# Optimization experiments

Hardware: AMD Instinct MI355X
Metric: run time of the kernel (lower is better)

The kernel has to match this reference:

```python
import jax, jax.numpy as jnp
import numpy as np

B, S, E, H = 4, 2048, 1024, 16
D = E // H
SCALE = np.sqrt(D).astype(np.float32)


def setup_inputs() -> dict:
    key = jax.random.key(0)
    ks = jax.random.split(key, 9)
    s = 1.0 / np.sqrt(E)
    return {
        "x": jax.random.normal(ks[0], (B, S, E), dtype=jnp.float32),
        "Wq": jax.random.uniform(ks[1], (E, E), jnp.float32, -s, s),
        "bq": jax.random.uniform(ks[2], (E,), jnp.float32, -s, s),
        "Wk": jax.random.uniform(ks[3], (E, E), jnp.float32, -s, s),
        "bk": jax.random.uniform(ks[4], (E,), jnp.float32, -s, s),
        "Wv": jax.random.uniform(ks[5], (E, E), jnp.float32, -s, s),
        "bv": jax.random.uniform(ks[6], (E,), jnp.float32, -s, s),
        "Wo": jax.random.uniform(ks[7], (E, E), jnp.float32, -s, s),
        "bo": jax.random.uniform(ks[8], (E,), jnp.float32, -s, s),
    }


def reference(x, Wq, bq, Wk, bk, Wv, bv, Wo, bo):
    # Linear projections (torch Linear: y = x @ W.T + b)
    q = x @ Wq.T + bq  # [B,S,E]
    k = x @ Wk.T + bk
    v = x @ Wv.T + bv
    # split heads -> [B,H,S,D]
    q = q.reshape(B, S, H, D).transpose(0, 2, 1, 3)
    k = k.reshape(B, S, H, D).transpose(0, 2, 1, 3)
    v = v.reshape(B, S, H, D).transpose(0, 2, 1, 3)
    scores = jnp.einsum("bhqd,bhkd->bhqk", q, k) / SCALE  # [B,H,S,S]
    attn = jax.nn.softmax(scores, axis=-1)  # dropout is identity at inference
    out = jnp.einsum("bhqk,bhkd->bhqd", attn, v)  # [B,H,S,D]
    out = out.transpose(0, 2, 1, 3).reshape(B, S, E)
    return out @ Wo.T + bo
```

## Files before the change

kernel.cpp:

```cpp
#include <hip/hip_runtime.h>
#include <math.h>

#define Bb 4
#define Ss 2048
#define Ee 1024
#define Hh 16
#define Dd 64

static constexpr int Mtot = Bb * Ss;
static constexpr size_t NK = (size_t)Ee * Ee;

typedef __bf16 bf16x8 __attribute__((ext_vector_type(8)));
typedef float  f32x16 __attribute__((ext_vector_type(16)));
typedef unsigned int uint32x2 __attribute__((ext_vector_type(2)));

extern "C" __device__ float __ocml_native_exp2_f32(float);

__device__ __forceinline__ unsigned short rne1(float x) {
  unsigned u = __float_as_uint(x);
  return (unsigned short)((u + 0x7FFFu + ((u >> 16) & 1u)) >> 16);
}
__device__ __forceinline__ short4 rne4(const float4 v) {
  short4 r;
  r.x = (short)rne1(v.x); r.y = (short)rne1(v.y);
  r.z = (short)rne1(v.z); r.w = (short)rne1(v.w);
  return r;
}

__global__ __launch_bounds__(256) void prep(const float* __restrict__ x,
                                            const float* __restrict__ wq,
                                            const float* __restrict__ wk,
                                            const float* __restrict__ wv,
                                            const float* __restrict__ wo,
                                            unsigned short* __restrict__ xb,
                                            unsigned short* __restrict__ wqkv,
                                            unsigned short* __restrict__ wob) {
  const int X4 = (int)((size_t)Mtot * Ee / 4);
  const int W4 = (int)(NK / 4);
  const int i = blockIdx.x * 256 + threadIdx.x;
  const float* src;
  unsigned short* dst;
  int off;
  if (i < X4) {
    src = x; dst = xb; off = i;
  } else {
    const int j = i - X4;
    const int seg = j >> 18;
    off = j & (W4 - 1);
    if (seg == 0)      { src = wq; dst = wqkv; }
    else if (seg == 1) { src = wk; dst = wqkv + NK; }
    else if (seg == 2) { src = wv; dst = wqkv + 2 * NK; }
    else               { src = wo; dst = wob; }
  }
  float4 v = ((const float4*)src)[off];
  ((short4*)dst)[off] = rne4(v);
}

__device__ __forceinline__ void gemm_core(const unsigned short* __restrict__ A,
                                          const unsigned short* __restrict__ W,
                                          unsigned short* sm, int bm, int bn,
                                          int tid, f32x16 acc[2][2]) {
  unsigned short* sA = sm;
  unsigned short* sW = sm + 9216;
  const int r  = tid >> 1;
  const int ch = (tid & 1) << 5;
  const int lane = tid & 63, w = tid >> 6;
  const int wm = (w & 1) << 6, wn = (w >> 1) << 6;
  const int m32 = lane & 31, g = lane >> 5;

  const unsigned short* A0 = A + (size_t)(bm + r) * Ee + ch;
  const unsigned short* W0 = W + (size_t)(bn + r) * Ee + ch;
  const int so = r * 72 + ch;

  for (int k0 = 0; k0 < Ee; k0 += 64) {
    uint4 a0 = *(const uint4*)(A0 + k0);
    uint4 a1 = *(const uint4*)(A0 + k0 + 8);
    uint4 a2 = *(const uint4*)(A0 + k0 + 16);
    uint4 a3 = *(const uint4*)(A0 + k0 + 24);
    uint4 w0 = *(const uint4*)(W0 + k0);
    uint4 w1 = *(const uint4*)(W0 + k0 + 8);
    uint4 w2 = *(const uint4*)(W0 + k0 + 16);
    uint4 w3 = *(const uint4*)(W0 + k0 + 24);
    __syncthreads();
    *(uint4*)(sA + so)      = a0; *(uint4*)(sA + so + 8)  = a1;
    *(uint4*)(sA + so + 16) = a2; *(uint4*)(sA + so + 24) = a3;
    *(uint4*)(sW + so)      = w0; *(uint4*)(sW + so + 8)  = w1;
    *(uint4*)(sW + so + 16) = w2; *(uint4*)(sW + so + 24) = w3;
    __syncthreads();
#pragma unroll
    for (int kk = 0; kk < 64; kk += 16) {
      const int kc = kk + (g << 3);
      bf16x8 af[2], wf[2];
#pragma unroll
      for (int s = 0; s < 2; ++s) {
        af[s] = *(const bf16x8*)(sA + (wm + (s << 5) + m32) * 72 + kc);
        wf[s] = *(const bf16x8*)(sW + (wn + (s << 5) + m32) * 72 + kc);
      }
#pragma unroll
      for (int si = 0; si < 2; ++si)
#pragma unroll
        for (int sj = 0; sj < 2; ++sj)
          acc[si][sj] = __builtin_amdgcn_mfma_f32_32x32x16_bf16(af[si], wf[sj], acc[si][sj], 0, 0, 0);
    }
  }
}


__global__ __launch_bounds__(256) void gemm_qkv(const unsigned short* __restrict__ xb,
                                                const unsigned short* __restrict__ wqkv,
                                                const float* __restrict__ bq,
                                                const float* __restrict__ bk,
                                                const float* __restrict__ bv,
                                                unsigned short* __restrict__ Qb,
                                                unsigned short* __restrict__ Kb,
                                                unsigned short* __restrict__ Vt) {
  __shared__ unsigned short sm[18432];
  f32x16 acc[2][2] = {};
  const int tid = threadIdx.x;
  const int bnIdx = blockIdx.x;
  const int bm = blockIdx.y << 7, bn = bnIdx << 7;
  gemm_core(xb, wqkv, sm, bm, bn, tid, acc);

  const int lane = tid & 63, w = tid >> 6;
  const int wm = (w & 1) << 6, wn = (w >> 1) << 6;
  const int m32 = lane & 31, g = lane >> 5;
  const int proj = bnIdx >> 3;
  const int cb   = (bnIdx & 7) << 7;
  const float* bp = proj == 0 ? bq : (proj == 1 ? bk : bv);
  const float SC = 0.18033688011112042f;

  if (proj == 2) {
    const int bmS = bm & (Ss - 1);
    const int b = bm >> 11;
#pragma unroll
    for (int si = 0; si < 2; ++si)
#pragma unroll
      for (int sj = 0; sj < 2; ++sj) {
        const int col = cb + wn + (sj << 5) + m32;
        const int hh = col >> 6, dd = col & 63;
        const float bvv = bp[col];
        unsigned short* vrow = Vt + ((size_t)((b * Hh + hh) * Dd + dd)) * Ss;
#pragma unroll
        for (int rq = 0; rq < 4; ++rq) {
          const int s0 = bmS + wm + (si << 5) + (g << 2) + (rq << 3);
          float4 v;
          v.x = acc[si][sj][rq * 4 + 0] + bvv;
          v.y = acc[si][sj][rq * 4 + 1] + bvv;
          v.z = acc[si][sj][rq * 4 + 2] + bvv;
          v.w = acc[si][sj][rq * 4 + 3] + bvv;
          *(short4*)(vrow + s0) = rne4(v);
        }
      }
  } else {
    unsigned short* dst = proj == 0 ? Qb : Kb;
    const float sc = proj == 0 ? SC : 1.0f;
#pragma unroll
    for (int si = 0; si < 2; ++si)
#pragma unroll
      for (int sj = 0; sj < 2; ++sj) {
        const int col = cb + wn + (sj << 5) + m32;
        const int hh = col >> 6, dd = col & 63;
        const float bvv = bp[col];
#pragma unroll
        for (int reg = 0; reg < 16; ++reg) {
          const int row = bm + wm + (si << 5) + (g << 2) + (reg & 3) + ((reg >> 2) << 3);
          const int b = row >> 11, s = row & (Ss - 1);
          dst[((size_t)((b * Hh + hh) * Ss + s)) * Dd + dd] =
              rne1((acc[si][sj][reg] + bvv) * sc);
        }
      }
  }
}

__global__ __launch_bounds__(256) void gemm_out(const unsigned short* __restrict__ Ab,
                                                const unsigned short* __restrict__ Wb,
                                                const float* __restrict__ bias,
                                                float* __restrict__ C) {
  __shared__ unsigned short sm[18432];
  f32x16 acc[2][2] = {};
  const int tid = threadIdx.x;
  const int bm = blockIdx.y << 7, bn = blockIdx.x << 7;
  gemm_core(Ab, Wb, sm, bm, bn, tid, acc);
  const int lane = tid & 63, w = tid >> 6;
  const int wm = (w & 1) << 6, wn = (w >> 1) << 6;
  const int m32 = lane & 31, g = lane >> 5;
#pragma unroll
  for (int si = 0; si < 2; ++si)
#pragma unroll
    for (int sj = 0; sj < 2; ++sj) {
      const int col = bn + wn + (sj << 5) + m32;
      const float bv = bias[col];
#pragma unroll
      for (int reg = 0; reg < 16; ++reg) {
        const int row = bm + wm + (si << 5) + (g << 2) + (reg & 3) + ((reg >> 2) << 3);
        C[(size_t)row * Ee + col] = acc[si][sj][reg] + bv;
      }
    }
}

__global__ __launch_bounds__(256) void flash_mfma(const unsigned short* __restrict__ Qb,
                                                  const unsigned short* __restrict__ Kb,
                                                  const unsigned short* __restrict__ Vt,
                                                  unsigned short* __restrict__ Ob) {
  __shared__ unsigned short smem[9216];
  unsigned short* Kh = smem;
  unsigned short* Vh = smem + 4608;
  const int tid = threadIdx.x;
  const int lane = tid & 63, w = tid >> 6;
  const int m32 = lane & 31, g = lane >> 5;
  const int qt = blockIdx.y << 7;
  const int bh = blockIdx.x;

  const size_t ph = (size_t)bh * Ss * Dd;
  const unsigned short* qp = Qb + ph + (size_t)(qt + (w << 5) + m32) * Dd + (g << 3);
  bf16x8 qf[4];
#pragma unroll
  for (int c = 0; c < 4; ++c) qf[c] = *(const bf16x8*)(qp + (c << 4));

  union { unsigned short us[8]; bf16x8 v; } onesu;
#pragma unroll
  for (int i = 0; i < 8; ++i) onesu.us[i] = 0x3F80;
  const bf16x8 ones = onesu.v;

  const int sr = tid >> 2;
  const int sc = (tid & 3) << 4;
  const unsigned short* kg = Kb + ph + (size_t)sr * Dd + sc;
  const unsigned short* vg = Vt + (size_t)bh * Dd * Ss + (size_t)sr * Ss + sc;
  const int so = sr * 72 + sc;

  uint4 k0 = *(const uint4*)(kg);
  uint4 k1 = *(const uint4*)(kg + 8);
  uint4 v0 = *(const uint4*)(vg);
  uint4 v1 = *(const uint4*)(vg + 8);

  f32x16 acc_o[2] = {};
  f32x16 acc_l = {};

  for (int kt = 0; kt < Ss; kt += 64) {
    __syncthreads();
    *(uint4*)(&Kh[so]) = k0; *(uint4*)(&Kh[so + 8]) = k1;
    *(uint4*)(&Vh[so]) = v0; *(uint4*)(&Vh[so + 8]) = v1;
    __syncthreads();
    if (kt + 64 < Ss) {
      const unsigned short* kg2 = kg + (size_t)(kt + 64) * Dd;
      const unsigned short* vg2 = vg + (kt + 64);
      k0 = *(const uint4*)(kg2);
      k1 = *(const uint4*)(kg2 + 8);
      v0 = *(const uint4*)(vg2);
      v1 = *(const uint4*)(vg2 + 8);
    }

    float p[2][16];
#pragma unroll
    for (int mt = 0; mt < 2; ++mt) {
      f32x16 a = {};
#pragma unroll
      for (int c = 0; c < 4; ++c) {
        bf16x8 kf = *(const bf16x8*)(&Kh[((mt << 5) + m32) * 72 + (c << 4) + (g << 3)]);
        a = __builtin_amdgcn_mfma_f32_32x32x16_bf16(kf, qf[c], a, 0, 0, 0);
      }
#pragma unroll
      for (int r = 0; r < 16; ++r) p[mt][r] = a[r];
    }
#pragma unroll
    for (int mt = 0; mt < 2; ++mt)
#pragma unroll
      for (int r = 0; r < 16; ++r)
        p[mt][r] = __ocml_native_exp2_f32(p[mt][r]);

#pragma unroll
    for (int c = 0; c < 4; ++c) {
      const int mt = c >> 1, b8 = (c & 1) << 3;
      unsigned dw0 = __builtin_amdgcn_perm(__float_as_uint(p[mt][b8 + 1]), __float_as_uint(p[mt][b8 + 0]), 0x07060302u);
      unsigned dw1 = __builtin_amdgcn_perm(__float_as_uint(p[mt][b8 + 3]), __float_as_uint(p[mt][b8 + 2]), 0x07060302u);
      unsigned dw2 = __builtin_amdgcn_perm(__float_as_uint(p[mt][b8 + 5]), __float_as_uint(p[mt][b8 + 4]), 0x07060302u);
      unsigned dw3 = __builtin_amdgcn_perm(__float_as_uint(p[mt][b8 + 7]), __float_as_uint(p[mt][b8 + 6]), 0x07060302u);
      const uint32x2 s02 = __builtin_amdgcn_permlane32_swap(dw0, dw2, false, false);
      const uint32x2 s13 = __builtin_amdgcn_permlane32_swap(dw1, dw3, false, false);
      union { unsigned u[4]; bf16x8 v; } pf;
      pf.u[0] = s02[0];
      pf.u[1] = s13[0];
      pf.u[2] = s02[1];
      pf.u[3] = s13[1];
#pragma unroll
      for (int dt = 0; dt < 2; ++dt) {
        bf16x8 vf = *(const bf16x8*)(&Vh[((dt << 5) + m32) * 72 + (c << 4) + (g << 3)]);
        acc_o[dt] = __builtin_amdgcn_mfma_f32_32x32x16_bf16(vf, pf.v, acc_o[dt], 0, 0, 0);
      }
      acc_l = __builtin_amdgcn_mfma_f32_32x32x16_bf16(ones, pf.v, acc_l, 0, 0, 0);
    }
  }

  const float inv = 1.0f / acc_l[0];
  const int q = (w << 5) + m32;
  unsigned short* Of = smem;
  __syncthreads();
#pragma unroll
  for (int dt = 0; dt < 2; ++dt)
#pragma unroll
    for (int r = 0; r < 16; ++r) {
      const int d = (dt << 5) + (g << 2) + (r & 3) + ((r >> 2) << 3);
      Of[q * 72 + d] = rne1(acc_o[dt][r] * inv);
    }
  __syncthreads();
  const int orow = tid >> 1, oc = (tid & 1) << 5;
  const int bq = bh >> 4, hh = bh & 15;
  const size_t obase = ((size_t)(bq * Ss + qt + orow)) * Ee + hh * Dd + oc;
#pragma unroll
  for (int i = 0; i < 2; ++i)
    *(uint4*)(Ob + obase + (i << 3)) = *(const uint4*)(&Of[orow * 72 + oc + (i << 3)]);
#pragma unroll
  for (int i = 2; i < 4; ++i)
    *(uint4*)(Ob + obase + (i << 3)) = *(const uint4*)(&Of[orow * 72 + oc + (i << 3)]);
}

extern "C" void kernel_launch(void* const* d_in, const int* in_sizes, int n_in,
                              void* d_out, int out_size, void* d_ws, size_t ws_size,
                              hipStream_t stream) {
  const float* x  = (const float*)d_in[0];
  const float* Wq = (const float*)d_in[1];
  const float* bq = (const float*)d_in[2];
  const float* Wk = (const float*)d_in[3];
  const float* bk = (const float*)d_in[4];
  const float* Wv = (const float*)d_in[5];
  const float* bv = (const float*)d_in[6];
  const float* Wo = (const float*)d_in[7];
  const float* bo = (const float*)d_in[8];
  float* out = (float*)d_out;

  const size_t nX = (size_t)Mtot * Ee;
  unsigned short* xb   = (unsigned short*)d_ws;
  unsigned short* qb   = xb + nX;
  unsigned short* kb   = qb + nX;
  unsigned short* vt   = kb + nX;
  unsigned short* ob   = vt + nX;
  unsigned short* wqkv = ob + nX;
  unsigned short* wob  = wqkv + 3 * NK;

  const int total4 = (int)(nX / 4 + NK);
  prep<<<total4 / 256, 256, 0, stream>>>(x, Wq, Wk, Wv, Wo, xb, wqkv, wob);

  gemm_qkv<<<dim3(3 * Ee / 128, Mtot / 128), 256, 0, stream>>>(xb, wqkv, bq, bk, bv, qb, kb, vt);

  flash_mfma<<<dim3(Bb * Hh, Ss / 128), 256, 0, stream>>>(qb, kb, vt, ob);

  gemm_out<<<dim3(Ee / 128, Mtot / 128), 256, 0, stream>>>(ob, wob, bo, out);
}
```

Baseline: 287.0 us.

## Double flash attention query tile to 256 rows with 512-thread blocks

The flash attention kernel now processes 256 query rows per block using 8 waves instead of 128 rows with 4 waves. Each K/V tile loaded into shared memory is therefore reused by twice as many queries, halving global K/V traffic, and each thread loads half as much per tile. The output staging through shared memory is split into two passes because the staging buffer holds only 128 rows. The grid shrinks to 512 blocks, which may lower occupancy flexibility and increases barrier cost per block.

```diff
diff --git a/kernel.cpp b/kernel.cpp
--- a/kernel.cpp
+++ b/kernel.cpp
@@ -198,7 +198,7 @@
     }
 }
 
-__global__ __launch_bounds__(256) void flash_mfma(const unsigned short* __restrict__ Qb,
+__global__ __launch_bounds__(512) void flash_mfma(const unsigned short* __restrict__ Qb,
                                                   const unsigned short* __restrict__ Kb,
                                                   const unsigned short* __restrict__ Vt,
                                                   unsigned short* __restrict__ Ob) {
@@ -208,7 +208,7 @@
   const int tid = threadIdx.x;
   const int lane = tid & 63, w = tid >> 6;
   const int m32 = lane & 31, g = lane >> 5;
-  const int qt = blockIdx.y << 7;
+  const int qt = blockIdx.y << 8;
   const int bh = blockIdx.x;
 
   const size_t ph = (size_t)bh * Ss * Dd;
@@ -222,32 +222,26 @@
   for (int i = 0; i < 8; ++i) onesu.us[i] = 0x3F80;
   const bf16x8 ones = onesu.v;
 
-  const int sr = tid >> 2;
-  const int sc = (tid & 3) << 4;
+  const int sr = tid >> 3;
+  const int sc = (tid & 7) << 3;
   const unsigned short* kg = Kb + ph + (size_t)sr * Dd + sc;
   const unsigned short* vg = Vt + (size_t)bh * Dd * Ss + (size_t)sr * Ss + sc;
   const int so = sr * 72 + sc;
 
   uint4 k0 = *(const uint4*)(kg);
-  uint4 k1 = *(const uint4*)(kg + 8);
   uint4 v0 = *(const uint4*)(vg);
-  uint4 v1 = *(const uint4*)(vg + 8);
 
   f32x16 acc_o[2] = {};
   f32x16 acc_l = {};
 
   for (int kt = 0; kt < Ss; kt += 64) {
     __syncthreads();
-    *(uint4*)(&Kh[so]) = k0; *(uint4*)(&Kh[so + 8]) = k1;
-    *(uint4*)(&Vh[so]) = v0; *(uint4*)(&Vh[so + 8]) = v1;
+    *(uint4*)(&Kh[so]) = k0;
+    *(uint4*)(&Vh[so]) = v0;
     __syncthreads();
     if (kt + 64 < Ss) {
-      const unsigned short* kg2 = kg + (size_t)(kt + 64) * Dd;
-      const unsigned short* vg2 = vg + (kt + 64);
-      k0 = *(const uint4*)(kg2);
-      k1 = *(const uint4*)(kg2 + 8);
-      v0 = *(const uint4*)(vg2);
-      v1 = *(const uint4*)(vg2 + 8);
+      k0 = *(const uint4*)(kg + (size_t)(kt + 64) * Dd);
+      v0 = *(const uint4*)(vg + (kt + 64));
     }
 
     float p[2][16];
@@ -292,26 +286,27 @@
   }
 
   const float inv = 1.0f / acc_l[0];
-  const int q = (w << 5) + m32;
+  const int qh = ((w & 3) << 5) + m32;
   unsigned short* Of = smem;
-  __syncthreads();
-#pragma unroll
-  for (int dt = 0; dt < 2; ++dt)
-#pragma unroll
-    for (int r = 0; r < 16; ++r) {
-      const int d = (dt << 5) + (g << 2) + (r & 3) + ((r >> 2) << 3);
-      Of[q * 72 + d] = rne1(acc_o[dt][r] * inv);
-    }
-  __syncthreads();
-  const int orow = tid >> 1, oc = (tid & 1) << 5;
   const int bq = bh >> 4, hh = bh & 15;
-  const size_t obase = ((size_t)(bq * Ss + qt + orow)) * Ee + hh * Dd + oc;
-#pragma unroll
-  for (int i = 0; i < 2; ++i)
-    *(uint4*)(Ob + obase + (i << 3)) = *(const uint4*)(&Of[orow * 72 + oc + (i << 3)]);
-#pragma unroll
-  for (int i = 2; i < 4; ++i)
-    *(uint4*)(Ob + obase + (i << 3)) = *(const uint4*)(&Of[orow * 72 + oc + (i << 3)]);
+  const int orow = tid >> 2, oc = (tid & 3) << 4;
+#pragma unroll
+  for (int h = 0; h < 2; ++h) {
+    __syncthreads();
+    if ((w >> 2) == h) {
+#pragma unroll
+      for (int dt = 0; dt < 2; ++dt)
+#pragma unroll
+        for (int r = 0; r < 16; ++r) {
+          const int d = (dt << 5) + (g << 2) + (r & 3) + ((r >> 2) << 3);
+          Of[qh * 72 + d] = rne1(acc_o[dt][r] * inv);
+        }
+    }
+    __syncthreads();
+    const size_t obase = ((size_t)(bq * Ss + qt + (h << 7) + orow)) * Ee + hh * Dd + oc;
+    *(uint4*)(Ob + obase)     = *(const uint4*)(&Of[orow * 72 + oc]);
+    *(uint4*)(Ob + obase + 8) = *(const uint4*)(&Of[orow * 72 + oc + 8]);
+  }
 }
 
 extern "C" void kernel_launch(void* const* d_in, const int* in_sizes, int n_in,
@@ -342,7 +337,7 @@
 
   gemm_qkv<<<dim3(3 * Ee / 128, Mtot / 128), 256, 0, stream>>>(xb, wqkv, bq, bk, bv, qb, kb, vt);
 
-  flash_mfma<<<dim3(Bb * Hh, Ss / 128), 256, 0, stream>>>(qb, kb, vt, ob);
+  flash_mfma<<<dim3(Bb * Hh, Ss / 256), 512, 0, stream>>>(qb, kb, vt, ob);
 
   gemm_out<<<dim3(Ee / 128, Mtot / 128), 256, 0, stream>>>(ob, wob, bo, out);
 }
```

After: 272.8 us. 5.0% less time.
